# Kernel tuning notes

Measured on AMD Instinct MI355X. Metric: run time of the kernel, lower is better.

## Reference

```python
import jax, jax.numpy as jnp
import numpy as np

B, S, E = 8, 4096, 512
QKV, H = 512, 8
D = QKV // H  # head_dim = 64
EPS = 1e-6


def setup_inputs() -> dict:
    key = jax.random.key(0)
    ks = jax.random.split(key, 9)
    sc_in = 1.0 / np.sqrt(E)
    sc_qkv = 1.0 / np.sqrt(QKV)
    # Linear weights stored as [in, out] so y = x @ W + b (equivalent to torch x @ W_t.T + b)
    return {
        "x": jax.random.normal(ks[0], (B, S, E), dtype=jnp.float32),
        "Wq": jax.random.uniform(ks[1], (E, QKV), jnp.float32, -sc_in, sc_in),
        "bq": jax.random.uniform(ks[2], (QKV,), jnp.float32, -sc_in, sc_in),
        "Wk": jax.random.uniform(ks[3], (E, QKV), jnp.float32, -sc_in, sc_in),
        "bk": jax.random.uniform(ks[4], (QKV,), jnp.float32, -sc_in, sc_in),
        "Wv": jax.random.uniform(ks[5], (E, QKV), jnp.float32, -sc_in, sc_in),
        "bv": jax.random.uniform(ks[6], (QKV,), jnp.float32, -sc_in, sc_in),
        "Wo": jax.random.uniform(ks[7], (QKV, E), jnp.float32, -sc_qkv, sc_qkv),
        "bo": jax.random.uniform(ks[8], (E,), jnp.float32, -sc_qkv, sc_qkv),
    }


def feature_map(t):
    # elu(x) + 1 (always positive features)
    return jax.nn.elu(t) + 1.0


def reference(x, Wq, bq, Wk, bk, Wv, bv, Wo, bo):
    bs, seqlen, _ = x.shape
    q = (x @ Wq + bq).reshape(bs, seqlen, H, D)
    k = (x @ Wk + bk).reshape(bs, seqlen, H, D)
    v = (x @ Wv + bv).reshape(bs, seqlen, H, D)
    q = feature_map(q)
    k = feature_map(k)
    # kv: [n, h, m, d] -- per-head outer-product accumulation over sequence
    kv = jnp.einsum('nshd,nshm->nhmd', k, v)
    # normalizer z: [n, l, h]
    z = 1.0 / (jnp.einsum('nlhd,nhd->nlh', q, k.sum(axis=1)) + EPS)
    out = jnp.einsum('nlhd,nhmd,nlh->nlhm', q, kv, z)
    out = out.reshape(bs, seqlen, QKV)
    return out @ Wo + bo
```

## Files before the change

### kernel.cpp

```cpp
#include <hip/hip_runtime.h>
#include <hip/hip_bf16.h>


typedef __bf16 bf16x8 __attribute__((ext_vector_type(8)));
typedef float  f32x4  __attribute__((ext_vector_type(4)));

__device__ __forceinline__ float b2f(unsigned short u) {
    unsigned int x = ((unsigned int)u) << 16;
    return __builtin_bit_cast(float, x);
}
__device__ __forceinline__ unsigned short f2b(float f) {
    unsigned int u = __builtin_bit_cast(unsigned int, f);
    unsigned int r = (u + 0x7FFFu + ((u >> 16) & 1u)) >> 16;
    return (unsigned short)r;
}
__device__ __forceinline__ void load_lds16(const unsigned short* g, unsigned short* l) {
    __builtin_amdgcn_global_load_lds(
        (const __attribute__((address_space(1))) void*)g,
        (__attribute__((address_space(3))) void*)l, 16, 0, 0);
}

__global__ void prep_kernel(const float* __restrict__ x,
                            const float* __restrict__ w0, const float* __restrict__ w1,
                            const float* __restrict__ w2, const float* __restrict__ w3,
                            unsigned short* __restrict__ xb, unsigned short* __restrict__ wt) {
    __shared__ float tile[64][65];
    int t = threadIdx.x;
    if (blockIdx.x >= 256) {
        int i = (blockIdx.x - 256) * 256 + t;
        float4 v = ((const float4*)x)[i];
        ushort4 o;
        o.x = f2b(v.x); o.y = f2b(v.y); o.z = f2b(v.z); o.w = f2b(v.w);
        ((ushort4*)xb)[i] = o;
        return;
    }
    int idx = blockIdx.x;
    int bz = idx >> 6, by = (idx >> 3) & 7, bx = idx & 7;
    const float* src = (bz == 0) ? w0 : (bz == 1) ? w1 : (bz == 2) ? w2 : w3;
    unsigned short* dst = wt + (size_t)bz * 512 * 512;
    int rb = by * 64, cb = bx * 64;
    #pragma unroll
    for (int i = 0; i < 16; i++) {
        int c = t + i * 256; int r = c >> 6, cc = c & 63;
        tile[r][cc] = src[(rb + r) * 512 + cb + cc];
    }
    __syncthreads();
    #pragma unroll
    for (int i = 0; i < 16; i++) {
        int c = t + i * 256; int r = c >> 6, cc = c & 63;
        dst[(cb + r) * 512 + rb + cc] = f2b(tile[cc][r]);
    }
}

__global__ __launch_bounds__(256, 4) void gemm_qkv_kernel(
        const unsigned short* __restrict__ xb, const unsigned short* __restrict__ wt,
        const float* __restrict__ bq, const float* __restrict__ bk, const float* __restrict__ bv,
        unsigned short* __restrict__ qb, unsigned short* __restrict__ kT,
        unsigned short* __restrict__ vT) {
    int g = blockIdx.x;
    int xcd = g & 7, slot = g >> 3;
    int mtile = xcd * 32 + slot / 12;
    int tn = slot % 12;
    int tensor = tn >> 2, ntile = tn & 3;
    const unsigned short* Bt = wt + (size_t)tensor * 512 * 512;
    const float* bias = tensor == 0 ? bq : tensor == 1 ? bk : bv;
    bool act = tensor < 2;

    __shared__ __align__(16) unsigned short sA[128 * 64];
    __shared__ __align__(16) unsigned short sB[128 * 64];
    const int tid  = threadIdx.x;
    const int wave = tid >> 6, lane = tid & 63;
    const int wm = wave >> 1, wn = wave & 1;
    const int quad = lane >> 4, l16 = lane & 15;
    const int mbase = mtile * 128, nbase = ntile * 128;
    const int rsub = lane >> 3;
    const int coff = (((lane & 7) ^ rsub) << 3);

    f32x4 acc[4][4];
    #pragma unroll
    for (int i = 0; i < 4; i++)
        #pragma unroll
        for (int j = 0; j < 4; j++) acc[i][j] = (f32x4){0.f, 0.f, 0.f, 0.f};

    for (int kb = 0; kb < 512; kb += 64) {
        #pragma unroll
        for (int t = 0; t < 4; t++) {
            int r0 = t * 32 + wave * 8;
            load_lds16(&xb[(size_t)(mbase + r0 + rsub) * 512 + kb + coff], &sA[r0 * 64]);
            load_lds16(&Bt[(size_t)(nbase + r0 + rsub) * 512 + kb + coff], &sB[r0 * 64]);
        }
        __syncthreads();
        #pragma unroll
        for (int ko = 0; ko < 64; ko += 32) {
            bf16x8 af[4], bfr[4];
            int pg = ((quad + (ko >> 3)) ^ (l16 & 7)) << 3;
            #pragma unroll
            for (int f = 0; f < 4; f++)
                af[f] = *(const bf16x8*)&sA[(wm * 64 + f * 16 + l16) * 64 + pg];
            #pragma unroll
            for (int f = 0; f < 4; f++)
                bfr[f] = *(const bf16x8*)&sB[(wn * 64 + f * 16 + l16) * 64 + pg];
            #pragma unroll
            for (int i = 0; i < 4; i++)
                #pragma unroll
                for (int j = 0; j < 4; j++)
                    acc[i][j] = __builtin_amdgcn_mfma_f32_16x16x32_bf16(af[i], bfr[j], acc[i][j], 0, 0, 0);
        }
        __syncthreads();
    }
    if (tensor == 0) {
        #pragma unroll
        for (int i = 0; i < 4; i++)
            #pragma unroll
            for (int j = 0; j < 4; j++) {
                int gcol = nbase + wn * 64 + j * 16 + l16;
                float bv = bias[gcol];
                #pragma unroll
                for (int r = 0; r < 4; r++) {
                    int grow = mbase + wm * 64 + i * 16 + quad * 4 + r;
                    float v = acc[i][j][r] + bv;
                    v = v > 0.f ? v + 1.f : __expf(v);
                    qb[(size_t)grow * 512 + gcol] = f2b(v);
                }
            }
    } else {
        unsigned short* T = (tensor == 1) ? kT : vT;
        #pragma unroll
        for (int i = 0; i < 4; i++)
            #pragma unroll
            for (int j = 0; j < 4; j++) {
                int gcol = nbase + wn * 64 + j * 16 + l16;
                int h = gcol >> 6, d = gcol & 63;
                float bv = bias[gcol];
                int grow0 = mbase + wm * 64 + i * 16 + quad * 4;
                int b = grow0 >> 12, s0 = grow0 & 4095;
                ushort4 o;
                #pragma unroll
                for (int r = 0; r < 4; r++) {
                    float v = acc[i][j][r] + bv;
                    if (act) v = v > 0.f ? v + 1.f : __expf(v);
                    ((unsigned short*)&o)[r] = f2b(v);
                }
                *(ushort4*)&T[(((size_t)b * 8 + h) * 64 + d) * 4096 + s0] = o;
            }
    }
}

__global__ __launch_bounds__(256, 4) void kv_kernel(
        const unsigned short* __restrict__ kT, const unsigned short* __restrict__ vT,
        float* __restrict__ kvp, float* __restrict__ ksp) {
    int bh = blockIdx.x >> 4, sc = blockIdx.x & 15;
    const int tid = threadIdx.x;
    const int wave = tid >> 6, lane = tid & 63;
    const int wm = wave >> 1, wn = wave & 1;
    const int quad = lane >> 4, l16 = lane & 15;
    const int rsub = lane >> 3;
    const int coff = (((lane & 7) ^ rsub) << 3);
    __shared__ __align__(16) unsigned short sV[64 * 64];
    __shared__ __align__(16) unsigned short sK[64 * 64];
    __shared__ float sKs[256];

    f32x4 acc[2][2];
    #pragma unroll
    for (int i = 0; i < 2; i++)
        #pragma unroll
        for (int j = 0; j < 2; j++) acc[i][j] = (f32x4){0.f, 0.f, 0.f, 0.f};
    float ks = 0.f;
    const int dks = tid >> 2, sgks = tid & 3;
    size_t base = (size_t)bh * 64 * 4096 + sc * 256;

    for (int kb = 0; kb < 4; kb++) {
        int s0 = kb * 64;
        #pragma unroll
        for (int t = 0; t < 2; t++) {
            int r0 = t * 32 + wave * 8;
            load_lds16(&vT[base + (size_t)(r0 + rsub) * 4096 + s0 + coff], &sV[r0 * 64]);
            load_lds16(&kT[base + (size_t)(r0 + rsub) * 4096 + s0 + coff], &sK[r0 * 64]);
        }
        __syncthreads();
        #pragma unroll
        for (int gi = 0; gi < 2; gi++) {
            int gg = sgks * 2 + gi;
            int pg = ((gg ^ (dks & 7)) << 3);
            uint4 w = *(const uint4*)&sK[dks * 64 + pg];
            const unsigned int* wp = (const unsigned int*)&w;
            #pragma unroll
            for (int i2 = 0; i2 < 4; i2++) {
                ks += __builtin_bit_cast(float, wp[i2] << 16);
                ks += __builtin_bit_cast(float, wp[i2] & 0xFFFF0000u);
            }
        }
        #pragma unroll
        for (int ko = 0; ko < 64; ko += 32) {
            bf16x8 af[2], bfr[2];
            int pg = ((quad + (ko >> 3)) ^ (l16 & 7)) << 3;
            #pragma unroll
            for (int f = 0; f < 2; f++)
                af[f] = *(const bf16x8*)&sV[(wm * 32 + f * 16 + l16) * 64 + pg];
            #pragma unroll
            for (int f = 0; f < 2; f++)
                bfr[f] = *(const bf16x8*)&sK[(wn * 32 + f * 16 + l16) * 64 + pg];
            #pragma unroll
            for (int i = 0; i < 2; i++)
                #pragma unroll
                for (int j = 0; j < 2; j++)
                    acc[i][j] = __builtin_amdgcn_mfma_f32_16x16x32_bf16(af[i], bfr[j], acc[i][j], 0, 0, 0);
        }
        __syncthreads();
    }
    float* kvout = kvp + ((size_t)sc * 64 + bh) * 4096;
    #pragma unroll
    for (int i = 0; i < 2; i++)
        #pragma unroll
        for (int j = 0; j < 2; j++)
            #pragma unroll
            for (int r = 0; r < 4; r++) {
                int m = wm * 32 + i * 16 + quad * 4 + r;
                int d = wn * 32 + j * 16 + l16;
                kvout[m * 64 + d] = acc[i][j][r];
            }
    sKs[tid] = ks;
    __syncthreads();
    if (tid < 64)
        ksp[((size_t)sc * 64 + bh) * 64 + tid] =
            sKs[tid * 4] + sKs[tid * 4 + 1] + sKs[tid * 4 + 2] + sKs[tid * 4 + 3];
}

__global__ __launch_bounds__(256) void mid_kernel(
        const float* __restrict__ kvp, const float* __restrict__ ksp,
        const unsigned short* __restrict__ qb,
        unsigned short* __restrict__ kvb, float* __restrict__ zb) {
    int bh = blockIdx.x >> 3, chunk = blockIdx.x & 7;
    int b = bh >> 3, h = bh & 7;
    int tid = threadIdx.x;
    __shared__ float sKsum[64];
    if (tid < 64) {
        float s = 0.f;
        #pragma unroll
        for (int sc = 0; sc < 16; sc++) s += ksp[((size_t)sc * 64 + bh) * 64 + tid];
        sKsum[tid] = s;
    }
    __syncthreads();
    int seg = tid & 7, rsub = tid >> 3;
    float ks8[8];
    #pragma unroll
    for (int j = 0; j < 8; j++) ks8[j] = sKsum[seg * 8 + j];
    #pragma unroll
    for (int p = 0; p < 16; p++) {
        int row = chunk * 512 + p * 32 + rsub;
        uint4 w = *(const uint4*)&qb[((size_t)(b * 4096 + row)) * 512 + h * 64 + seg * 8];
        const unsigned int* qp = (const unsigned int*)&w;
        float d = 0.f;
        #pragma unroll
        for (int i = 0; i < 4; i++) {
            d += __builtin_bit_cast(float, qp[i] << 16)        * ks8[2*i];
            d += __builtin_bit_cast(float, qp[i] & 0xFFFF0000u) * ks8[2*i+1];
        }
        d += __shfl_xor(d, 1, 64);
        d += __shfl_xor(d, 2, 64);
        d += __shfl_xor(d, 4, 64);
        if (seg == 0) zb[h * 32768 + b * 4096 + row] = 1.f / (d + 1e-6f);
    }
    if (chunk == 0) {
        #pragma unroll
        for (int i = 0; i < 4; i++) {
            int idx = (tid + i * 256) * 4;
            float s0 = 0.f, s1 = 0.f, s2 = 0.f, s3 = 0.f;
            #pragma unroll
            for (int sc = 0; sc < 16; sc++) {
                float4 v = *(const float4*)&kvp[((size_t)sc * 64 + bh) * 4096 + idx];
                s0 += v.x; s1 += v.y; s2 += v.z; s3 += v.w;
            }
            ushort4 o; o.x = f2b(s0); o.y = f2b(s1); o.z = f2b(s2); o.w = f2b(s3);
            *(ushort4*)&kvb[(size_t)bh * 4096 + idx] = o;
        }
    }
}

__global__ __launch_bounds__(256, 2) void fused_out_kernel(
        const unsigned short* __restrict__ qb,
        const unsigned short* __restrict__ kvb, const float* __restrict__ zb,
        const unsigned short* __restrict__ wto, const float* __restrict__ bo,
        float* __restrict__ out) {
    int g = blockIdx.x;
    int xcd = g & 7, slot = g >> 3;
    int mtile = xcd * 32 + (slot >> 2);
    int ntile = slot & 3;

    __shared__ __align__(16) unsigned short sQ[128 * 64];
    __shared__ __align__(16) unsigned short sWo[128 * 64];
    __shared__ __align__(16) unsigned short sKV[64 * 64];
    __shared__ __align__(16) unsigned short sO1[128 * 64];
    __shared__ float sZ[128];
    const int tid  = threadIdx.x;
    const int wave = tid >> 6, lane = tid & 63;
    const int wm = wave >> 1, wn = wave & 1;
    const int quad = lane >> 4, l16 = lane & 15;
    const int mbase = mtile * 128, nbase = ntile * 128;
    const int b = mtile >> 5;
    const int rsub = lane >> 3;
    const int coff = (((lane & 7) ^ rsub) << 3);

    f32x4 accm[4][4];
    #pragma unroll
    for (int i = 0; i < 4; i++)
        #pragma unroll
        for (int j = 0; j < 4; j++) accm[i][j] = (f32x4){0.f, 0.f, 0.f, 0.f};

    for (int h = 0; h < 8; h++) {
        #pragma unroll
        for (int t = 0; t < 4; t++) {
            int r0 = t * 32 + wave * 8;
            load_lds16(&qb[(size_t)(mbase + r0 + rsub) * 512 + h * 64 + coff], &sQ[r0 * 64]);
            load_lds16(&wto[(size_t)(nbase + r0 + rsub) * 512 + h * 64 + coff], &sWo[r0 * 64]);
        }
        #pragma unroll
        for (int t = 0; t < 2; t++) {
            int r0 = t * 32 + wave * 8;
            load_lds16(&kvb[(size_t)(b * 8 + h) * 4096 + (r0 + rsub) * 64 + coff], &sKV[r0 * 64]);
        }
        if (tid < 128) sZ[tid] = zb[h * 32768 + mbase + tid];
        __syncthreads();
        f32x4 acco[4][2];
        #pragma unroll
        for (int f = 0; f < 4; f++)
            #pragma unroll
            for (int j = 0; j < 2; j++) acco[f][j] = (f32x4){0.f, 0.f, 0.f, 0.f};
        #pragma unroll
        for (int ko = 0; ko < 64; ko += 32) {
            bf16x8 af[4], bfr[2];
            int pg = ((quad + (ko >> 3)) ^ (l16 & 7)) << 3;
            #pragma unroll
            for (int f = 0; f < 4; f++)
                af[f] = *(const bf16x8*)&sQ[(wm * 64 + f * 16 + l16) * 64 + pg];
            #pragma unroll
            for (int j = 0; j < 2; j++)
                bfr[j] = *(const bf16x8*)&sKV[(wn * 32 + j * 16 + l16) * 64 + pg];
            #pragma unroll
            for (int f = 0; f < 4; f++)
                #pragma unroll
                for (int j = 0; j < 2; j++)
                    acco[f][j] = __builtin_amdgcn_mfma_f32_16x16x32_bf16(af[f], bfr[j], acco[f][j], 0, 0, 0);
        }
        #pragma unroll
        for (int f = 0; f < 4; f++)
            #pragma unroll
            for (int j = 0; j < 2; j++)
                #pragma unroll
                for (int r = 0; r < 4; r++) {
                    int row = wm * 64 + f * 16 + quad * 4 + r;
                    int col = wn * 32 + j * 16 + l16;
                    float v = acco[f][j][r] * sZ[row];
                    int grp = col >> 3;
                    sO1[row * 64 + ((grp ^ (row & 7)) << 3) + (col & 7)] = f2b(v);
                }
        __syncthreads();
        #pragma unroll
        for (int ko = 0; ko < 64; ko += 32) {
            bf16x8 af[4], bfr[4];
            int pg = ((quad + (ko >> 3)) ^ (l16 & 7)) << 3;
            #pragma unroll
            for (int f = 0; f < 4; f++)
                af[f] = *(const bf16x8*)&sO1[(wm * 64 + f * 16 + l16) * 64 + pg];
            #pragma unroll
            for (int f = 0; f < 4; f++)
                bfr[f] = *(const bf16x8*)&sWo[(wn * 64 + f * 16 + l16) * 64 + pg];
            #pragma unroll
            for (int i = 0; i < 4; i++)
                #pragma unroll
                for (int j = 0; j < 4; j++)
                    accm[i][j] = __builtin_amdgcn_mfma_f32_16x16x32_bf16(af[i], bfr[j], accm[i][j], 0, 0, 0);
        }
        __syncthreads();
    }
    #pragma unroll
    for (int i = 0; i < 4; i++)
        #pragma unroll
        for (int j = 0; j < 4; j++) {
            int gcol = nbase + wn * 64 + j * 16 + l16;
            float bv = bo[gcol];
            #pragma unroll
            for (int r = 0; r < 4; r++) {
                int grow = mbase + wm * 64 + i * 16 + quad * 4 + r;
                out[(size_t)grow * 512 + gcol] = accm[i][j][r] + bv;
            }
        }
}

extern "C" void kernel_launch(void* const* d_in, const int* in_sizes, int n_in,
                              void* d_out, int out_size, void* d_ws, size_t ws_size,
                              hipStream_t stream) {
    const float* x  = (const float*)d_in[0];
    const float* Wq = (const float*)d_in[1];
    const float* bq = (const float*)d_in[2];
    const float* Wk = (const float*)d_in[3];
    const float* bk = (const float*)d_in[4];
    const float* Wv = (const float*)d_in[5];
    const float* bv = (const float*)d_in[6];
    const float* Wo = (const float*)d_in[7];
    const float* bo = (const float*)d_in[8];
    float* out = (float*)d_out;

    char* wsb = (char*)d_ws;
    char* ob  = (char*)d_out;
    unsigned short* vT  = (unsigned short*)ob;
    unsigned short* xb  = (unsigned short*)(ob + 33554432ull);
    float*          kvp = (float*)(ob + 33554432ull);
    unsigned short* qb  = (unsigned short*)wsb;
    unsigned short* kT  = (unsigned short*)(wsb + 33554432ull);
    unsigned short* wt  = (unsigned short*)(wsb + 67108864ull);
    float*          ksp = (float*)(wsb + 69206016ull);
    unsigned short* kvb = (unsigned short*)(wsb + 69468160ull);
    float*          zb  = (float*)(wsb + 69992448ull);

    prep_kernel<<<16640, 256, 0, stream>>>(x, Wq, Wk, Wv, Wo, xb, wt);
    gemm_qkv_kernel<<<3072, 256, 0, stream>>>(xb, wt, bq, bk, bv, qb, kT, vT);
    kv_kernel<<<1024, 256, 0, stream>>>(kT, vT, kvp, ksp);
    mid_kernel<<<512, 256, 0, stream>>>(kvp, ksp, qb, kvb, zb);
    fused_out_kernel<<<1024, 256, 0, stream>>>(qb, kvb, zb,
            wt + 3ull * 512 * 512, bo, out);
}
```

Before: 269.9 us.

## Use 256x256 tiles with double-buffered async LDS pipeline in QKV GEMM

Rewrites the QKV projection GEMM to use 512-thread blocks computing 256x256 output tiles instead of 128x128, which halves how often A and B are reloaded per output. Global-to-LDS loads are double-buffered and issued in interleaved stages between MFMA groups. Explicit waitcnt/barrier placement and s_setprio let memory transfers overlap with matrix math. In exchange it uses 128KB of LDS and large accumulator register files, so occupancy drops to one block per CU. The grid also shrinks to 768 blocks, which may leave parts of the GPU underused.

```diff
diff --git a/kernel.cpp b/kernel.cpp
--- a/kernel.cpp
+++ b/kernel.cpp
@@ -52,72 +52,144 @@
     }
 }
 
-__global__ __launch_bounds__(256, 4) void gemm_qkv_kernel(
+__global__ __launch_bounds__(512, 1) void gemm_qkv_kernel(
         const unsigned short* __restrict__ xb, const unsigned short* __restrict__ wt,
         const float* __restrict__ bq, const float* __restrict__ bk, const float* __restrict__ bv,
         unsigned short* __restrict__ qb, unsigned short* __restrict__ kT,
         unsigned short* __restrict__ vT) {
+    __shared__ __align__(16) unsigned short lds[65536];
     int g = blockIdx.x;
     int xcd = g & 7, slot = g >> 3;
-    int mtile = xcd * 32 + slot / 12;
-    int tn = slot % 12;
-    int tensor = tn >> 2, ntile = tn & 3;
+    int mtile = xcd * 16 + slot / 6;
+    int tn = slot % 6;
+    int tensor = tn >> 1, ntile = tn & 1;
     const unsigned short* Bt = wt + (size_t)tensor * 512 * 512;
     const float* bias = tensor == 0 ? bq : tensor == 1 ? bk : bv;
     bool act = tensor < 2;
 
-    __shared__ __align__(16) unsigned short sA[128 * 64];
-    __shared__ __align__(16) unsigned short sB[128 * 64];
     const int tid  = threadIdx.x;
     const int wave = tid >> 6, lane = tid & 63;
-    const int wm = wave >> 1, wn = wave & 1;
+    const int wm = wave >> 2, wn = wave & 3;
     const int quad = lane >> 4, l16 = lane & 15;
-    const int mbase = mtile * 128, nbase = ntile * 128;
     const int rsub = lane >> 3;
     const int coff = (((lane & 7) ^ rsub) << 3);
-
-    f32x4 acc[4][4];
-    #pragma unroll
-    for (int i = 0; i < 4; i++)
+    const int mbase = mtile * 256, nbase = ntile * 256;
+    const int pg0 = ((quad)     ^ (l16 & 7)) << 3;
+    const int pg1 = ((quad + 4) ^ (l16 & 7)) << 3;
+
+    auto stageA = [&](int ts, int h) {
+        int tc = ts < 7 ? ts : 7;
+        unsigned short* dst = &lds[(ts & 1) * 32768 + h * 8192];
+        int rb = mbase + h * 128, kb = tc * 64;
+        #pragma unroll
+        for (int rnd = 0; rnd < 2; rnd++) {
+            int r0 = rnd * 64 + wave * 8;
+            load_lds16(&xb[(size_t)(rb + r0 + rsub) * 512 + kb + coff], &dst[r0 * 64]);
+        }
+    };
+    auto stageB = [&](int ts, int h) {
+        int tc = ts < 7 ? ts : 7;
+        unsigned short* dst = &lds[(ts & 1) * 32768 + 16384 + h * 8192];
+        int rb = nbase + h * 128, kb = tc * 64;
+        #pragma unroll
+        for (int rnd = 0; rnd < 2; rnd++) {
+            int r0 = rnd * 64 + wave * 8;
+            load_lds16(&Bt[(size_t)(rb + r0 + rsub) * 512 + kb + coff], &dst[r0 * 64]);
+        }
+    };
+
+    f32x4 acc[8][4];
+    #pragma unroll
+    for (int i = 0; i < 8; i++)
         #pragma unroll
         for (int j = 0; j < 4; j++) acc[i][j] = (f32x4){0.f, 0.f, 0.f, 0.f};
 
-    for (int kb = 0; kb < 512; kb += 64) {
-        #pragma unroll
-        for (int t = 0; t < 4; t++) {
-            int r0 = t * 32 + wave * 8;
-            load_lds16(&xb[(size_t)(mbase + r0 + rsub) * 512 + kb + coff], &sA[r0 * 64]);
-            load_lds16(&Bt[(size_t)(nbase + r0 + rsub) * 512 + kb + coff], &sB[r0 * 64]);
-        }
-        __syncthreads();
-        #pragma unroll
-        for (int ko = 0; ko < 64; ko += 32) {
-            bf16x8 af[4], bfr[4];
-            int pg = ((quad + (ko >> 3)) ^ (l16 & 7)) << 3;
-            #pragma unroll
-            for (int f = 0; f < 4; f++)
-                af[f] = *(const bf16x8*)&sA[(wm * 64 + f * 16 + l16) * 64 + pg];
-            #pragma unroll
-            for (int f = 0; f < 4; f++)
-                bfr[f] = *(const bf16x8*)&sB[(wn * 64 + f * 16 + l16) * 64 + pg];
-            #pragma unroll
-            for (int i = 0; i < 4; i++)
-                #pragma unroll
-                for (int j = 0; j < 4; j++)
-                    acc[i][j] = __builtin_amdgcn_mfma_f32_16x16x32_bf16(af[i], bfr[j], acc[i][j], 0, 0, 0);
-        }
-        __syncthreads();
-    }
+    stageA(0, 0); stageA(0, 1);
+    stageB(0, 0); stageB(0, 1);
+    stageB(1, 0); stageB(1, 1);
+    asm volatile("s_waitcnt vmcnt(4)" ::: "memory");
+    __builtin_amdgcn_s_barrier();
+
+    #pragma unroll 2
+    for (int t = 0; t < 8; ++t) {
+        const unsigned short* A = &lds[(t & 1) * 32768];
+        const unsigned short* Bl = &lds[(t & 1) * 32768 + 16384];
+        bf16x8 af[4][2], bf[4][2];
+        #pragma unroll
+        for (int i = 0; i < 4; i++) {
+            af[i][0] = *(const bf16x8*)&A[(wm * 128 + i * 16 + l16) * 64 + pg0];
+            af[i][1] = *(const bf16x8*)&A[(wm * 128 + i * 16 + l16) * 64 + pg1];
+        }
+        #pragma unroll
+        for (int j = 0; j < 4; j++) {
+            bf[j][0] = *(const bf16x8*)&Bl[(wn * 64 + j * 16 + l16) * 64 + pg0];
+            bf[j][1] = *(const bf16x8*)&Bl[(wn * 64 + j * 16 + l16) * 64 + pg1];
+        }
+        stageA(t + 1, 0);
+        __builtin_amdgcn_s_setprio(1);
+        #pragma unroll
+        for (int i = 0; i < 4; i++)
+            #pragma unroll
+            for (int j = 0; j < 2; j++) {
+                acc[i][j] = __builtin_amdgcn_mfma_f32_16x16x32_bf16(af[i][0], bf[j][0], acc[i][j], 0, 0, 0);
+                acc[i][j] = __builtin_amdgcn_mfma_f32_16x16x32_bf16(af[i][1], bf[j][1], acc[i][j], 0, 0, 0);
+            }
+        __builtin_amdgcn_s_setprio(0);
+        __builtin_amdgcn_s_barrier();
+        stageA(t + 1, 1);
+        __builtin_amdgcn_s_setprio(1);
+        #pragma unroll
+        for (int i = 0; i < 4; i++)
+            #pragma unroll
+            for (int j = 2; j < 4; j++) {
+                acc[i][j] = __builtin_amdgcn_mfma_f32_16x16x32_bf16(af[i][0], bf[j][0], acc[i][j], 0, 0, 0);
+                acc[i][j] = __builtin_amdgcn_mfma_f32_16x16x32_bf16(af[i][1], bf[j][1], acc[i][j], 0, 0, 0);
+            }
+        __builtin_amdgcn_s_setprio(0);
+        asm volatile("s_waitcnt lgkmcnt(0)" ::: "memory");
+        __builtin_amdgcn_sched_barrier(0);
+        __builtin_amdgcn_s_barrier();
+        bf16x8 a2[4][2];
+        #pragma unroll
+        for (int i = 0; i < 4; i++) {
+            a2[i][0] = *(const bf16x8*)&A[(wm * 128 + (i + 4) * 16 + l16) * 64 + pg0];
+            a2[i][1] = *(const bf16x8*)&A[(wm * 128 + (i + 4) * 16 + l16) * 64 + pg1];
+        }
+        stageB(t + 2, 0);
+        __builtin_amdgcn_s_setprio(1);
+        #pragma unroll
+        for (int i = 0; i < 4; i++)
+            #pragma unroll
+            for (int j = 0; j < 2; j++) {
+                acc[i + 4][j] = __builtin_amdgcn_mfma_f32_16x16x32_bf16(a2[i][0], bf[j][0], acc[i + 4][j], 0, 0, 0);
+                acc[i + 4][j] = __builtin_amdgcn_mfma_f32_16x16x32_bf16(a2[i][1], bf[j][1], acc[i + 4][j], 0, 0, 0);
+            }
+        __builtin_amdgcn_s_setprio(0);
+        __builtin_amdgcn_s_barrier();
+        stageB(t + 2, 1);
+        __builtin_amdgcn_s_setprio(1);
+        #pragma unroll
+        for (int i = 0; i < 4; i++)
+            #pragma unroll
+            for (int j = 2; j < 4; j++) {
+                acc[i + 4][j] = __builtin_amdgcn_mfma_f32_16x16x32_bf16(a2[i][0], bf[j][0], acc[i + 4][j], 0, 0, 0);
+                acc[i + 4][j] = __builtin_amdgcn_mfma_f32_16x16x32_bf16(a2[i][1], bf[j][1], acc[i + 4][j], 0, 0, 0);
+            }
+        __builtin_amdgcn_s_setprio(0);
+        asm volatile("s_waitcnt vmcnt(4)" ::: "memory");
+        __builtin_amdgcn_s_barrier();
+    }
+
     if (tensor == 0) {
         #pragma unroll
-        for (int i = 0; i < 4; i++)
+        for (int i = 0; i < 8; i++)
             #pragma unroll
             for (int j = 0; j < 4; j++) {
                 int gcol = nbase + wn * 64 + j * 16 + l16;
                 float bv = bias[gcol];
                 #pragma unroll
                 for (int r = 0; r < 4; r++) {
-                    int grow = mbase + wm * 64 + i * 16 + quad * 4 + r;
+                    int grow = mbase + wm * 128 + i * 16 + quad * 4 + r;
                     float v = acc[i][j][r] + bv;
                     v = v > 0.f ? v + 1.f : __expf(v);
                     qb[(size_t)grow * 512 + gcol] = f2b(v);
@@ -126,13 +198,13 @@
     } else {
         unsigned short* T = (tensor == 1) ? kT : vT;
         #pragma unroll
-        for (int i = 0; i < 4; i++)
+        for (int i = 0; i < 8; i++)
             #pragma unroll
             for (int j = 0; j < 4; j++) {
                 int gcol = nbase + wn * 64 + j * 16 + l16;
                 int h = gcol >> 6, d = gcol & 63;
                 float bv = bias[gcol];
-                int grow0 = mbase + wm * 64 + i * 16 + quad * 4;
+                int grow0 = mbase + wm * 128 + i * 16 + quad * 4;
                 int b = grow0 >> 12, s0 = grow0 & 4095;
                 ushort4 o;
                 #pragma unroll
@@ -414,7 +486,7 @@
     float*          zb  = (float*)(wsb + 69992448ull);
 
     prep_kernel<<<16640, 256, 0, stream>>>(x, Wq, Wk, Wv, Wo, xb, wt);
-    gemm_qkv_kernel<<<3072, 256, 0, stream>>>(xb, wt, bq, bk, bv, qb, kT, vT);
+    gemm_qkv_kernel<<<768, 512, 0, stream>>>(xb, wt, bq, bk, bv, qb, kT, vT);
     kv_kernel<<<1024, 256, 0, stream>>>(kT, vT, kvp, ksp);
     mid_kernel<<<512, 256, 0, stream>>>(kvp, ksp, qb, kvb, zb);
     fused_out_kernel<<<1024, 256, 0, stream>>>(qb, kvb, zb,
```

Measured after the change: 268.7 us. About the same (-0.4%).

## Fuse key-sum into QKV GEMM epilogue and compute normalizer in output kernel

Applied to the files above, without the earlier changes.

The per-column sum of the feature-mapped keys is now accumulated in the QKV GEMM epilogue through wave shuffles and global atomics, replacing the LDS-based key sum in kv_kernel. The mid kernel no longer reads all of Q to build the normalizer z; the fused output kernel instead computes z per head from the Q tile already staged in LDS. This removes a full extra pass over Q and a z buffer round-trip through memory. In exchange it adds atomics and an extra barrier in the output kernel, and the key sum is now taken over fp32 values before the bf16 cast, so summation order is no longer deterministic.

```diff
diff --git a/kernel.cpp b/kernel.cpp
--- a/kernel.cpp
+++ b/kernel.cpp
@@ -23,7 +23,8 @@
 __global__ void prep_kernel(const float* __restrict__ x,
                             const float* __restrict__ w0, const float* __restrict__ w1,
                             const float* __restrict__ w2, const float* __restrict__ w3,
-                            unsigned short* __restrict__ xb, unsigned short* __restrict__ wt) {
+                            unsigned short* __restrict__ xb, unsigned short* __restrict__ wt,
+                            float* __restrict__ ksg) {
     __shared__ float tile[64][65];
     int t = threadIdx.x;
     if (blockIdx.x >= 256) {
@@ -35,6 +36,7 @@
         return;
     }
     int idx = blockIdx.x;
+    if (idx < 16) ksg[idx * 256 + t] = 0.f;
     int bz = idx >> 6, by = (idx >> 3) & 7, bx = idx & 7;
     const float* src = (bz == 0) ? w0 : (bz == 1) ? w1 : (bz == 2) ? w2 : w3;
     unsigned short* dst = wt + (size_t)bz * 512 * 512;
@@ -56,7 +58,7 @@
         const unsigned short* __restrict__ xb, const unsigned short* __restrict__ wt,
         const float* __restrict__ bq, const float* __restrict__ bk, const float* __restrict__ bv,
         unsigned short* __restrict__ qb, unsigned short* __restrict__ kT,
-        unsigned short* __restrict__ vT) {
+        unsigned short* __restrict__ vT, float* __restrict__ ksg) {
     int g = blockIdx.x;
     int xcd = g & 7, slot = g >> 3;
     int mtile = xcd * 32 + slot / 12;
@@ -125,6 +127,7 @@
             }
     } else {
         unsigned short* T = (tensor == 1) ? kT : vT;
+        float csum[4] = {0.f, 0.f, 0.f, 0.f};
         #pragma unroll
         for (int i = 0; i < 4; i++)
             #pragma unroll
@@ -138,17 +141,30 @@
                 #pragma unroll
                 for (int r = 0; r < 4; r++) {
                     float v = acc[i][j][r] + bv;
-                    if (act) v = v > 0.f ? v + 1.f : __expf(v);
+                    if (act) { v = v > 0.f ? v + 1.f : __expf(v); csum[j] += v; }
                     ((unsigned short*)&o)[r] = f2b(v);
                 }
                 *(ushort4*)&T[(((size_t)b * 8 + h) * 64 + d) * 4096 + s0] = o;
             }
+        if (act) {
+            int b = mbase >> 12;
+            #pragma unroll
+            for (int j = 0; j < 4; j++) {
+                float s = csum[j];
+                s += __shfl_xor(s, 16, 64);
+                s += __shfl_xor(s, 32, 64);
+                if (quad == 0) {
+                    int gcol = nbase + wn * 64 + j * 16 + l16;
+                    atomicAdd(&ksg[b * 512 + gcol], s);
+                }
+            }
+        }
     }
 }
 
 __global__ __launch_bounds__(256, 4) void kv_kernel(
         const unsigned short* __restrict__ kT, const unsigned short* __restrict__ vT,
-        float* __restrict__ kvp, float* __restrict__ ksp) {
+        float* __restrict__ kvp) {
     int bh = blockIdx.x >> 4, sc = blockIdx.x & 15;
     const int tid = threadIdx.x;
     const int wave = tid >> 6, lane = tid & 63;
@@ -158,15 +174,12 @@
     const int coff = (((lane & 7) ^ rsub) << 3);
     __shared__ __align__(16) unsigned short sV[64 * 64];
     __shared__ __align__(16) unsigned short sK[64 * 64];
-    __shared__ float sKs[256];
 
     f32x4 acc[2][2];
     #pragma unroll
     for (int i = 0; i < 2; i++)
         #pragma unroll
         for (int j = 0; j < 2; j++) acc[i][j] = (f32x4){0.f, 0.f, 0.f, 0.f};
-    float ks = 0.f;
-    const int dks = tid >> 2, sgks = tid & 3;
     size_t base = (size_t)bh * 64 * 4096 + sc * 256;
 
     for (int kb = 0; kb < 4; kb++) {
@@ -179,18 +192,6 @@
         }
         __syncthreads();
         #pragma unroll
-        for (int gi = 0; gi < 2; gi++) {
-            int gg = sgks * 2 + gi;
-            int pg = ((gg ^ (dks & 7)) << 3);
-            uint4 w = *(const uint4*)&sK[dks * 64 + pg];
-            const unsigned int* wp = (const unsigned int*)&w;
-            #pragma unroll
-            for (int i2 = 0; i2 < 4; i2++) {
-                ks += __builtin_bit_cast(float, wp[i2] << 16);
-                ks += __builtin_bit_cast(float, wp[i2] & 0xFFFF0000u);
-            }
-        }
-        #pragma unroll
         for (int ko = 0; ko < 64; ko += 32) {
             bf16x8 af[2], bfr[2];
             int pg = ((quad + (ko >> 3)) ^ (l16 & 7)) << 3;
@@ -219,67 +220,26 @@
                 int d = wn * 32 + j * 16 + l16;
                 kvout[m * 64 + d] = acc[i][j][r];
             }
-    sKs[tid] = ks;
-    __syncthreads();
-    if (tid < 64)
-        ksp[((size_t)sc * 64 + bh) * 64 + tid] =
-            sKs[tid * 4] + sKs[tid * 4 + 1] + sKs[tid * 4 + 2] + sKs[tid * 4 + 3];
 }
 
 __global__ __launch_bounds__(256) void mid_kernel(
-        const float* __restrict__ kvp, const float* __restrict__ ksp,
-        const unsigned short* __restrict__ qb,
-        unsigned short* __restrict__ kvb, float* __restrict__ zb) {
-    int bh = blockIdx.x >> 3, chunk = blockIdx.x & 7;
-    int b = bh >> 3, h = bh & 7;
+        const float* __restrict__ kvp, unsigned short* __restrict__ kvb) {
+    int bh = blockIdx.x >> 2, part = blockIdx.x & 3;
     int tid = threadIdx.x;
-    __shared__ float sKsum[64];
-    if (tid < 64) {
-        float s = 0.f;
-        #pragma unroll
-        for (int sc = 0; sc < 16; sc++) s += ksp[((size_t)sc * 64 + bh) * 64 + tid];
-        sKsum[tid] = s;
-    }
-    __syncthreads();
-    int seg = tid & 7, rsub = tid >> 3;
-    float ks8[8];
-    #pragma unroll
-    for (int j = 0; j < 8; j++) ks8[j] = sKsum[seg * 8 + j];
-    #pragma unroll
-    for (int p = 0; p < 16; p++) {
-        int row = chunk * 512 + p * 32 + rsub;
-        uint4 w = *(const uint4*)&qb[((size_t)(b * 4096 + row)) * 512 + h * 64 + seg * 8];
-        const unsigned int* qp = (const unsigned int*)&w;
-        float d = 0.f;
-        #pragma unroll
-        for (int i = 0; i < 4; i++) {
-            d += __builtin_bit_cast(float, qp[i] << 16)        * ks8[2*i];
-            d += __builtin_bit_cast(float, qp[i] & 0xFFFF0000u) * ks8[2*i+1];
-        }
-        d += __shfl_xor(d, 1, 64);
-        d += __shfl_xor(d, 2, 64);
-        d += __shfl_xor(d, 4, 64);
-        if (seg == 0) zb[h * 32768 + b * 4096 + row] = 1.f / (d + 1e-6f);
-    }
-    if (chunk == 0) {
-        #pragma unroll
-        for (int i = 0; i < 4; i++) {
-            int idx = (tid + i * 256) * 4;
-            float s0 = 0.f, s1 = 0.f, s2 = 0.f, s3 = 0.f;
-            #pragma unroll
-            for (int sc = 0; sc < 16; sc++) {
-                float4 v = *(const float4*)&kvp[((size_t)sc * 64 + bh) * 4096 + idx];
-                s0 += v.x; s1 += v.y; s2 += v.z; s3 += v.w;
-            }
-            ushort4 o; o.x = f2b(s0); o.y = f2b(s1); o.z = f2b(s2); o.w = f2b(s3);
-            *(ushort4*)&kvb[(size_t)bh * 4096 + idx] = o;
-        }
-    }
+    int idx = (part * 256 + tid) * 4;
+    float s0 = 0.f, s1 = 0.f, s2 = 0.f, s3 = 0.f;
+    #pragma unroll
+    for (int sc = 0; sc < 16; sc++) {
+        float4 v = *(const float4*)&kvp[((size_t)sc * 64 + bh) * 4096 + idx];
+        s0 += v.x; s1 += v.y; s2 += v.z; s3 += v.w;
+    }
+    ushort4 o; o.x = f2b(s0); o.y = f2b(s1); o.z = f2b(s2); o.w = f2b(s3);
+    *(ushort4*)&kvb[(size_t)bh * 4096 + idx] = o;
 }
 
 __global__ __launch_bounds__(256, 2) void fused_out_kernel(
         const unsigned short* __restrict__ qb,
-        const unsigned short* __restrict__ kvb, const float* __restrict__ zb,
+        const unsigned short* __restrict__ kvb, const float* __restrict__ ksg,
         const unsigned short* __restrict__ wto, const float* __restrict__ bo,
         float* __restrict__ out) {
     int g = blockIdx.x;
@@ -291,6 +251,7 @@
     __shared__ __align__(16) unsigned short sWo[128 * 64];
     __shared__ __align__(16) unsigned short sKV[64 * 64];
     __shared__ __align__(16) unsigned short sO1[128 * 64];
+    __shared__ float sKsum[512];
     __shared__ float sZ[128];
     const int tid  = threadIdx.x;
     const int wave = tid >> 6, lane = tid & 63;
@@ -301,6 +262,9 @@
     const int rsub = lane >> 3;
     const int coff = (((lane & 7) ^ rsub) << 3);
 
+    sKsum[tid]       = ksg[b * 512 + tid];
+    sKsum[tid + 256] = ksg[b * 512 + 256 + tid];
+
     f32x4 accm[4][4];
     #pragma unroll
     for (int i = 0; i < 4; i++)
@@ -319,7 +283,26 @@
             int r0 = t * 32 + wave * 8;
             load_lds16(&kvb[(size_t)(b * 8 + h) * 4096 + (r0 + rsub) * 64 + coff], &sKV[r0 * 64]);
         }
-        if (tid < 128) sZ[tid] = zb[h * 32768 + mbase + tid];
+        __syncthreads();
+        {
+            int row = tid >> 1, half = tid & 1;
+            const float* ksh = &sKsum[h * 64];
+            float dsum = 0.f;
+            #pragma unroll
+            for (int g2 = 0; g2 < 4; g2++) {
+                int G = half * 4 + g2;
+                uint4 w = *(const uint4*)&sQ[row * 64 + ((G ^ (row & 7)) << 3)];
+                const unsigned int* qp = (const unsigned int*)&w;
+                #pragma unroll
+                for (int u = 0; u < 4; u++) {
+                    int c = G * 8 + u * 2;
+                    dsum += __builtin_bit_cast(float, qp[u] << 16)        * ksh[c];
+                    dsum += __builtin_bit_cast(float, qp[u] & 0xFFFF0000u) * ksh[c + 1];
+                }
+            }
+            dsum += __shfl_xor(dsum, 1, 64);
+            if (!half) sZ[row] = 1.f / (dsum + 1e-6f);
+        }
         __syncthreads();
         f32x4 acco[4][2];
         #pragma unroll
@@ -409,14 +392,13 @@
     unsigned short* qb  = (unsigned short*)wsb;
     unsigned short* kT  = (unsigned short*)(wsb + 33554432ull);
     unsigned short* wt  = (unsigned short*)(wsb + 67108864ull);
-    float*          ksp = (float*)(wsb + 69206016ull);
-    unsigned short* kvb = (unsigned short*)(wsb + 69468160ull);
-    float*          zb  = (float*)(wsb + 69992448ull);
-
-    prep_kernel<<<16640, 256, 0, stream>>>(x, Wq, Wk, Wv, Wo, xb, wt);
-    gemm_qkv_kernel<<<3072, 256, 0, stream>>>(xb, wt, bq, bk, bv, qb, kT, vT);
-    kv_kernel<<<1024, 256, 0, stream>>>(kT, vT, kvp, ksp);
-    mid_kernel<<<512, 256, 0, stream>>>(kvp, ksp, qb, kvb, zb);
-    fused_out_kernel<<<1024, 256, 0, stream>>>(qb, kvb, zb,
+    unsigned short* kvb = (unsigned short*)(wsb + 69206016ull);
+    float*          ksg = (float*)(wsb + 69730304ull);
+
+    prep_kernel<<<16640, 256, 0, stream>>>(x, Wq, Wk, Wv, Wo, xb, wt, ksg);
+    gemm_qkv_kernel<<<3072, 256, 0, stream>>>(xb, wt, bq, bk, bv, qb, kT, vT, ksg);
+    kv_kernel<<<1024, 256, 0, stream>>>(kT, vT, kvp);
+    mid_kernel<<<256, 256, 0, stream>>>(kvp, kvb);
+    fused_out_kernel<<<1024, 256, 0, stream>>>(qb, kvb, ksg,
             wt + 3ull * 512 * 512, bo, out);
 }
```

Result: faster. 259.8 us (-3.7%).
